# Kernel tuning notes

Hardware: AMD Instinct MI355X
Metric: run time of the kernel (lower is better)

## Reference

```python
import jax, jax.numpy as jnp
import numpy as np

HOP = jnp.array([0, 1, 4, 7, 2, 5, 8, 3, 6, 9, 11, 14, 10, 12, 15, 13, 16])
GRAPH = jnp.array([0, 1, 4, 7, 2, 5, 8, 3, 6, 9, 12, 10, 13, 15, 11, 14, 16])
D_MODEL, L, D_INNER, D_STATE, DT_RANK = 512, 17, 1024, 4, 32


def layernorm(x, w, b, eps=1e-5):
    mu = x.mean(-1, keepdims=True)
    var = ((x - mu) ** 2).mean(-1, keepdims=True)
    return (x - mu) * jax.lax.rsqrt(var + eps) * w + b


def setup_inputs() -> dict:
    key = jax.random.key(0)
    ks = jax.random.split(key, 9)
    B = 4096
    s = lambda k, shape: jax.random.normal(k, shape, jnp.float32) * 0.02
    # A_log init per mamba_ssm: log(1..d_state) repeated over d_inner
    A_log = jnp.log(jnp.broadcast_to(jnp.arange(1, D_STATE + 1, dtype=jnp.float32), (D_INNER, D_STATE)))
    return {
        "x": jax.random.normal(ks[0], (B, L, D_MODEL), jnp.float32),
        "bp_embed": s(ks[1], (1, 5, D_MODEL)),
        "ln_w": jnp.ones((D_MODEL,), jnp.float32),
        "ln_b": jnp.zeros((D_MODEL,), jnp.float32),
        "in_proj_w": s(ks[2], (2 * D_INNER, D_MODEL)),
        "conv_w": 1.0 + s(ks[3], (D_INNER,)),  # d_conv=1 depthwise conv == per-channel scale
        "conv_b": jnp.zeros((D_INNER,), jnp.float32),
        "x_proj_w": s(ks[4], (DT_RANK + 2 * D_STATE, D_INNER)),
        "dt_proj_w": s(ks[5], (D_INNER, DT_RANK)),
        "dt_proj_b": s(ks[6], (D_INNER,)) - 4.0,  # softplus-inverse-ish small dt init
        "A_log": A_log,
        "D": jnp.ones((D_INNER,), jnp.float32),
        "out_proj_w": s(ks[7], (D_MODEL, D_INNER)),
    }


def mamba(u, in_proj_w, conv_w, conv_b, x_proj_w, dt_proj_w, dt_proj_b, A_log, D, out_proj_w):
    # u: [B, L, d_model]
    xz = jnp.einsum('bld,ed->ble', u, in_proj_w)          # [B,L,2*d_inner]
    xm, z = jnp.split(xz, 2, axis=-1)
    xm = jax.nn.silu(xm * conv_w + conv_b)                 # d_conv=1 -> pointwise
    x_dbl = jnp.einsum('ble,fe->blf', xm, x_proj_w)        # [B,L,dt_rank+2*d_state]
    dt_r = x_dbl[..., :DT_RANK]
    Bm = x_dbl[..., DT_RANK:DT_RANK + D_STATE]
    Cm = x_dbl[..., DT_RANK + D_STATE:]
    dt = jax.nn.softplus(jnp.einsum('blr,er->ble', dt_r, dt_proj_w) + dt_proj_b)  # [B,L,d_inner]
    A = -jnp.exp(A_log)                                    # [d_inner,d_state]

    def step(h, inp):
        dt_t, B_t, C_t, x_t = inp                          # [B,di],[B,ds],[B,ds],[B,di]
        dA = jnp.exp(dt_t[..., None] * A)                  # [B,di,ds]
        h = dA * h + (dt_t * x_t)[..., None] * B_t[:, None, :]
        y = jnp.einsum('bes,bs->be', h, C_t)
        return h, y

    bsz = u.shape[0]
    h0 = jnp.zeros((bsz, D_INNER, D_STATE), u.dtype)
    seq = (dt.transpose(1, 0, 2), Bm.transpose(1, 0, 2), Cm.transpose(1, 0, 2), xm.transpose(1, 0, 2))
    _, ys = jax.lax.scan(step, h0, seq)                    # ys: [L,B,d_inner]
    y = ys.transpose(1, 0, 2) + xm * D
    y = y * jax.nn.silu(z)
    return jnp.einsum('ble,de->bld', y, out_proj_w)


def reference(x, bp_embed, ln_w, ln_b, in_proj_w, conv_w, conv_b, x_proj_w,
              dt_proj_w, dt_proj_b, A_log, D, out_proj_w):
    bp = bp_embed
    x_bpe = jnp.concatenate([bp[:, :3], bp[:, :3], bp[:, :3], bp[:, :1],
                             bp[:, 3:], bp[:, :1], bp[:, 3:], bp[:, 3:]], axis=1)  # [1,17,dim]
    x_ssm = x[:, HOP, :] + x_bpe
    x_ssm = layernorm(x_ssm, ln_w, ln_b)
    x_ssm = mamba(x_ssm, in_proj_w, conv_w, conv_b, x_proj_w,
                  dt_proj_w, dt_proj_b, A_log, D, out_proj_w)
    return x + x_ssm[:, GRAPH, :]
```

## Files before the change

### kernel.cpp

```cpp
#include <hip/hip_runtime.h>

typedef unsigned short u16;
typedef unsigned int   u32;
typedef __bf16 bf16_t;
typedef bf16_t bf16x8 __attribute__((ext_vector_type(8)));
typedef float  f32x4  __attribute__((ext_vector_type(4)));

#define DEV static __device__ __forceinline__

__constant__ int c_HOP[17] = {0,1,4,7,2,5,8,3,6,9,11,14,10,12,15,13,16};
__constant__ int c_BPE[17] = {0,1,2,0,1,2,0,1,2,0,3,4,0,3,4,3,4};

DEV u16 f2bf(float f){
  u32 x = __builtin_bit_cast(u32, f);
  x += 0x7fffu + ((x >> 16) & 1u);
  return (u16)(x >> 16);
}
DEV float bf2f(u32 u){ return __builtin_bit_cast(float, u << 16); }
DEV float silu_f(float v){ return v / (1.f + __expf(-v)); }

DEV void gll16(const void* g, void* l){
  __builtin_amdgcn_global_load_lds((__attribute__((address_space(1))) void*)g,
                                   (__attribute__((address_space(3))) void*)l,
                                   16, 0, 0);
}

__global__ __launch_bounds__(256) void cvt4(
    const float* __restrict__ s0, u16* __restrict__ d0, int n0,
    const float* __restrict__ s1, u16* __restrict__ d1, int n1,
    const float* __restrict__ s2, u16* __restrict__ d2, int n2,
    const float* __restrict__ s3, u16* __restrict__ d3, int n3)
{
  int t = blockIdx.x * 256 + threadIdx.x;
  if (t < n0){ d0[t] = f2bf(s0[t]); return; }
  t -= n0; if (t < n1){ d1[t] = f2bf(s1[t]); return; }
  t -= n1; if (t < n2){ d2[t] = f2bf(s2[t]); return; }
  t -= n2; if (t < n3){ d3[t] = f2bf(s3[t]); }
}

__global__ __launch_bounds__(256) void ln_gather(
    const float* __restrict__ x, const float* __restrict__ bpe,
    const float* __restrict__ lnw, const float* __restrict__ lnb,
    u16* __restrict__ u)
{
  int tok = blockIdx.x;
  int b = tok / 17;
  int l = tok - b * 17;
  const float* xr = x   + ((size_t)b * 17 + c_HOP[l]) * 512;
  const float* br = bpe + (size_t)c_BPE[l] * 512;
  int tid = threadIdx.x;
  int d0 = tid * 2;
  float2 xv = *(const float2*)(xr + d0);
  float2 bv = *(const float2*)(br + d0);
  float v0 = xv.x + bv.x, v1 = xv.y + bv.y;

  __shared__ float red[8];
  float s = v0 + v1;
  #pragma unroll
  for (int o = 32; o; o >>= 1) s += __shfl_xor(s, o);
  if ((tid & 63) == 0) red[tid >> 6] = s;
  __syncthreads();
  float mu = (red[0] + red[1] + red[2] + red[3]) * (1.f / 512.f);
  float a0 = v0 - mu, a1 = v1 - mu;
  float q = a0 * a0 + a1 * a1;
  #pragma unroll
  for (int o = 32; o; o >>= 1) q += __shfl_xor(q, o);
  if ((tid & 63) == 0) red[4 + (tid >> 6)] = q;
  __syncthreads();
  float var = (red[4] + red[5] + red[6] + red[7]) * (1.f / 512.f);
  float rs = rsqrtf(var + 1e-5f);

  u16 o0 = f2bf(a0 * rs * lnw[d0]     + lnb[d0]);
  u16 o1 = f2bf(a1 * rs * lnw[d0 + 1] + lnb[d0 + 1]);
  u32 pack = (u32)o0 | ((u32)o1 << 16);
  *(u32*)(u + (size_t)tok * 512 + d0) = pack;
}

enum { EPI_SPLIT = 0, EPI_XDBL = 1, EPI_DT = 2, EPI_OUT = 3 };

template<int EPI>
__global__ __launch_bounds__(256) void gemm_bt(
    const u16* __restrict__ A, int lda,
    const u16* __restrict__ W, int nW, int K, int MT,
    u16* __restrict__ ob0, u16* __restrict__ ob1,
    const float* __restrict__ p0, const float* __restrict__ p1,
    const float* __restrict__ xres, float* __restrict__ fout)
{
  __shared__ u16 sA[128 * 32];
  __shared__ u16 sW[128 * 32];
  int bid = blockIdx.x;
  int mt = bid % MT, nt = bid / MT;
  int brow = mt * 128, bcol = nt * 128;
  int tid = threadIdx.x, lane = tid & 63, wid = tid >> 6;
  int wm = wid >> 1, wn = wid & 1;

  f32x4 acc[4][4] = {};

  int srow = tid >> 2;
  int sch  = tid & 3;

  for (int kt = 0; kt < K; kt += 32) {
    #pragma unroll
    for (int i = 0; i < 2; i++) {
      int r = i * 64 + srow;
      int c = sch ^ ((r >> 1) & 3);
      gll16(A + (size_t)(brow + r) * lda + kt + c * 8,
            (char*)sA + tid * 16 + i * 4096);
    }
    #pragma unroll
    for (int i = 0; i < 2; i++) {
      int r = i * 64 + srow;
      int wr = bcol + r; wr = (wr < nW) ? wr : 0;
      int c = sch ^ ((r >> 1) & 3);
      gll16(W + (size_t)wr * K + kt + c * 8,
            (char*)sW + tid * 16 + i * 4096);
    }
    __syncthreads();

    bf16x8 av[4], bv[4];
    #pragma unroll
    for (int mi = 0; mi < 4; mi++) {
      int r = wm * 64 + mi * 16 + (lane & 15);
      int c = (lane >> 4) ^ ((r >> 1) & 3);
      av[mi] = *(const bf16x8*)((const char*)sA + r * 64 + c * 16);
    }
    #pragma unroll
    for (int ni = 0; ni < 4; ni++) {
      int r = wn * 64 + ni * 16 + (lane & 15);
      int c = (lane >> 4) ^ ((r >> 1) & 3);
      bv[ni] = *(const bf16x8*)((const char*)sW + r * 64 + c * 16);
    }
    #pragma unroll
    for (int mi = 0; mi < 4; mi++)
      #pragma unroll
      for (int ni = 0; ni < 4; ni++)
        acc[mi][ni] = __builtin_amdgcn_mfma_f32_16x16x32_bf16(
            av[mi], bv[ni], acc[mi][ni], 0, 0, 0);
    __syncthreads();
  }

  int r4 = (lane >> 4) * 4;
  int cl = lane & 15;
  #pragma unroll
  for (int mi = 0; mi < 4; mi++) {
    #pragma unroll
    for (int ni = 0; ni < 4; ni++) {
      int col = bcol + wn * 64 + ni * 16 + cl;
      if (col >= nW) continue;
      #pragma unroll
      for (int rr = 0; rr < 4; rr++) {
        int row = brow + wm * 64 + mi * 16 + r4 + rr;
        float v = acc[mi][ni][rr];
        if constexpr (EPI == EPI_SPLIT) {
          if (col < 1024) {
            float t = v * p0[col] + p1[col];
            ob0[(size_t)row * 1024 + col] = f2bf(silu_f(t));
          } else {
            ob1[(size_t)row * 1024 + (col - 1024)] = f2bf(silu_f(v));
          }
        } else if constexpr (EPI == EPI_XDBL) {
          ob0[(size_t)row * 40 + col] = f2bf(v);
        } else if constexpr (EPI == EPI_DT) {
          float s = v + p0[col];
          float dtv = (s > 20.f) ? s : log1pf(__expf(s));
          ob0[(size_t)row * 1024 + col] = f2bf(dtv);
        } else {
          u32 rw = (u32)row;
          u32 b = rw / 17u;
          int gl = (int)(rw - b * 17u);
          size_t oi = ((size_t)b * 17 + c_HOP[gl]) * 512 + col;
          fout[oi] = xres[oi] + v;
        }
      }
    }
  }
}

__global__ __launch_bounds__(256) void scan_k(
    const u16* __restrict__ xm, const u16* __restrict__ zs,
    const u16* __restrict__ xdbl, u16* __restrict__ dty,
    const float* __restrict__ A_log, const float* __restrict__ Dp)
{
  int gid = blockIdx.x * 256 + threadIdx.x;
  int b = gid >> 10, e = gid & 1023;
  float A0 = -__expf(A_log[e * 4 + 0]);
  float A1 = -__expf(A_log[e * 4 + 1]);
  float A2 = -__expf(A_log[e * 4 + 2]);
  float A3 = -__expf(A_log[e * 4 + 3]);
  float Dv = Dp[e];
  float h0 = 0.f, h1 = 0.f, h2 = 0.f, h3 = 0.f;
  size_t base = (size_t)b * 17;
  for (int t = 0; t < 17; t++) {
    size_t tok = base + t;
    size_t idx = tok * 1024 + e;
    float dt = bf2f(dty[idx]);
    float xv = bf2f(xm[idx]);
    float zv = bf2f(zs[idx]);
    uint4 raw = *(const uint4*)(xdbl + tok * 40 + 32);
    float B0 = bf2f(raw.x & 0xffffu), B1 = bf2f(raw.x >> 16);
    float B2 = bf2f(raw.y & 0xffffu), B3 = bf2f(raw.y >> 16);
    float C0 = bf2f(raw.z & 0xffffu), C1 = bf2f(raw.z >> 16);
    float C2 = bf2f(raw.w & 0xffffu), C3 = bf2f(raw.w >> 16);
    float dx = dt * xv;
    h0 = __expf(dt * A0) * h0 + dx * B0;
    h1 = __expf(dt * A1) * h1 + dx * B1;
    h2 = __expf(dt * A2) * h2 + dx * B2;
    h3 = __expf(dt * A3) * h3 + dx * B3;
    float y = h0 * C0 + h1 * C1 + h2 * C2 + h3 * C3;
    dty[idx] = f2bf((y + xv * Dv) * zv);
  }
}

extern "C" void kernel_launch(void* const* d_in, const int* in_sizes, int n_in,
                              void* d_out, int out_size, void* d_ws, size_t ws_size,
                              hipStream_t stream) {
  const float* x     = (const float*)d_in[0];
  const float* bpe   = (const float*)d_in[1];
  const float* lnw   = (const float*)d_in[2];
  const float* lnb   = (const float*)d_in[3];
  const float* w_in  = (const float*)d_in[4];
  const float* convw = (const float*)d_in[5];
  const float* convb = (const float*)d_in[6];
  const float* w_xp  = (const float*)d_in[7];
  const float* w_dt  = (const float*)d_in[8];
  const float* b_dt  = (const float*)d_in[9];
  const float* A_log = (const float*)d_in[10];
  const float* Dp    = (const float*)d_in[11];
  const float* w_out = (const float*)d_in[12];
  float* out = (float*)d_out;

  u16* ws = (u16*)d_ws;
  u16* wb_in  = ws;
  u16* wb_out = wb_in  + 1048576;
  u16* wb_xp  = wb_out + 524288;
  u16* wb_dt  = wb_xp  + 40960;
  u16* xm     = wb_dt  + 32768;
  u16* zs     = xm     + 71303168;
  u16* xdbl   = zs     + 71303168;
  u16* dty    = xdbl   + 2785280;
  u16* u      = dty;

  const int MT = 544;

  cvt4<<<6432, 256, 0, stream>>>(w_in, wb_in, 1048576, w_out, wb_out, 524288,
                                 w_xp, wb_xp, 40960, w_dt, wb_dt, 32768);

  ln_gather<<<69632, 256, 0, stream>>>(x, bpe, lnw, lnb, u);

  gemm_bt<EPI_SPLIT><<<MT * 16, 256, 0, stream>>>(
      u, 512, wb_in, 2048, 512, MT, xm, zs, convw, convb, nullptr, nullptr);

  gemm_bt<EPI_XDBL><<<MT * 1, 256, 0, stream>>>(
      xm, 1024, wb_xp, 40, 1024, MT, xdbl, nullptr, nullptr, nullptr, nullptr, nullptr);

  gemm_bt<EPI_DT><<<MT * 8, 256, 0, stream>>>(
      xdbl, 40, wb_dt, 1024, 32, MT, dty, nullptr, b_dt, nullptr, nullptr, nullptr);

  scan_k<<<16384, 256, 0, stream>>>(xm, zs, xdbl, dty, A_log, Dp);

  gemm_bt<EPI_OUT><<<MT * 4, 256, 0, stream>>>(
      dty, 1024, wb_out, 512, 1024, MT, nullptr, nullptr, nullptr, nullptr, x, out);
}
```

Measured before the change: 962.8 us.

## Fuse x_proj, dt_proj and selective scan into per-batch kernel; remap GEMM blocks

Replaces the separate x_proj GEMM, dt_proj GEMM and scan kernels with one per-batch-row kernel. It computes x_dbl with MFMA, keeps x_dbl and dt in shared memory, then runs the scan, so the large dt tensor never goes through global memory. The remaining GEMMs get an XCD-aware block index remap (blockIdx&7 striping, with the n tile varying fastest). The SPLIT epilogue now packs two bf16 outputs per 32-bit store using a lane shuffle. Risks: the fused kernel uses about 53KB of LDS per block, which limits occupancy, and its x_proj loads read straight from global memory with no tiling.

```diff
diff --git a/kernel.cpp b/kernel.cpp
--- a/kernel.cpp
+++ b/kernel.cpp
@@ -76,20 +76,23 @@
   *(u32*)(u + (size_t)tok * 512 + d0) = pack;
 }
 
-enum { EPI_SPLIT = 0, EPI_XDBL = 1, EPI_DT = 2, EPI_OUT = 3 };
+enum { EPI_SPLIT = 0, EPI_OUT = 1 };
 
 template<int EPI>
 __global__ __launch_bounds__(256) void gemm_bt(
     const u16* __restrict__ A, int lda,
-    const u16* __restrict__ W, int nW, int K, int MT,
+    const u16* __restrict__ W, int K, int MT,
     u16* __restrict__ ob0, u16* __restrict__ ob1,
     const float* __restrict__ p0, const float* __restrict__ p1,
     const float* __restrict__ xres, float* __restrict__ fout)
 {
   __shared__ u16 sA[128 * 32];
   __shared__ u16 sW[128 * 32];
-  int bid = blockIdx.x;
-  int mt = bid % MT, nt = bid / MT;
+  int nwg = gridDim.x;
+  int cpx = nwg >> 3;
+  int wg = (blockIdx.x & 7) * cpx + (blockIdx.x >> 3);
+  int NT = nwg / MT;
+  int nt = wg % NT, mt = wg / NT;
   int brow = mt * 128, bcol = nt * 128;
   int tid = threadIdx.x, lane = tid & 63, wid = tid >> 6;
   int wm = wid >> 1, wn = wid & 1;
@@ -110,9 +113,8 @@
     #pragma unroll
     for (int i = 0; i < 2; i++) {
       int r = i * 64 + srow;
-      int wr = bcol + r; wr = (wr < nW) ? wr : 0;
       int c = sch ^ ((r >> 1) & 3);
-      gll16(W + (size_t)wr * K + kt + c * 8,
+      gll16(W + (size_t)(bcol + r) * K + kt + c * 8,
             (char*)sW + tid * 16 + i * 4096);
     }
     __syncthreads();
@@ -143,71 +145,156 @@
   int cl = lane & 15;
   #pragma unroll
   for (int mi = 0; mi < 4; mi++) {
+    int rowb = brow + wm * 64 + mi * 16 + r4;
     #pragma unroll
     for (int ni = 0; ni < 4; ni++) {
       int col = bcol + wn * 64 + ni * 16 + cl;
-      if (col >= nW) continue;
-      #pragma unroll
-      for (int rr = 0; rr < 4; rr++) {
-        int row = brow + wm * 64 + mi * 16 + r4 + rr;
-        float v = acc[mi][ni][rr];
-        if constexpr (EPI == EPI_SPLIT) {
-          if (col < 1024) {
-            float t = v * p0[col] + p1[col];
-            ob0[(size_t)row * 1024 + col] = f2bf(silu_f(t));
-          } else {
-            ob1[(size_t)row * 1024 + (col - 1024)] = f2bf(silu_f(v));
+      if constexpr (EPI == EPI_SPLIT) {
+        bool isx = (col < 1024);
+        float cw = isx ? p0[col] : 1.f;
+        float cb = isx ? p1[col] : 0.f;
+        float rv[4];
+        #pragma unroll
+        for (int rr = 0; rr < 4; rr++)
+          rv[rr] = silu_f(acc[mi][ni][rr] * cw + cb);
+        #pragma unroll
+        for (int rr = 0; rr < 4; rr++) {
+          float ov = __shfl_xor(rv[rr], 1);
+          if (!(lane & 1)) {
+            u32 pk = (u32)f2bf(rv[rr]) | ((u32)f2bf(ov) << 16);
+            size_t rowoff = (size_t)(rowb + rr) * 1024;
+            if (isx) *(u32*)(ob0 + rowoff + col) = pk;
+            else     *(u32*)(ob1 + rowoff + (col - 1024)) = pk;
           }
-        } else if constexpr (EPI == EPI_XDBL) {
-          ob0[(size_t)row * 40 + col] = f2bf(v);
-        } else if constexpr (EPI == EPI_DT) {
-          float s = v + p0[col];
-          float dtv = (s > 20.f) ? s : log1pf(__expf(s));
-          ob0[(size_t)row * 1024 + col] = f2bf(dtv);
-        } else {
+        }
+      } else {
+        #pragma unroll
+        for (int rr = 0; rr < 4; rr++) {
+          int row = rowb + rr;
           u32 rw = (u32)row;
           u32 b = rw / 17u;
           int gl = (int)(rw - b * 17u);
           size_t oi = ((size_t)b * 17 + c_HOP[gl]) * 512 + col;
-          fout[oi] = xres[oi] + v;
+          fout[oi] = xres[oi] + acc[mi][ni][rr];
         }
       }
     }
   }
 }
 
-__global__ __launch_bounds__(256) void scan_k(
+__global__ __launch_bounds__(256) void mamba_mid(
     const u16* __restrict__ xm, const u16* __restrict__ zs,
-    const u16* __restrict__ xdbl, u16* __restrict__ dty,
-    const float* __restrict__ A_log, const float* __restrict__ Dp)
+    const u16* __restrict__ wxp, const u16* __restrict__ wdt,
+    const float* __restrict__ bdt, const float* __restrict__ A_log,
+    const float* __restrict__ Dp, u16* __restrict__ y)
 {
-  int gid = blockIdx.x * 256 + threadIdx.x;
-  int b = gid >> 10, e = gid & 1023;
-  float A0 = -__expf(A_log[e * 4 + 0]);
-  float A1 = -__expf(A_log[e * 4 + 1]);
-  float A2 = -__expf(A_log[e * 4 + 2]);
-  float A3 = -__expf(A_log[e * 4 + 3]);
-  float Dv = Dp[e];
-  float h0 = 0.f, h1 = 0.f, h2 = 0.f, h3 = 0.f;
-  size_t base = (size_t)b * 17;
-  for (int t = 0; t < 17; t++) {
-    size_t tok = base + t;
-    size_t idx = tok * 1024 + e;
-    float dt = bf2f(dty[idx]);
-    float xv = bf2f(xm[idx]);
-    float zv = bf2f(zs[idx]);
-    uint4 raw = *(const uint4*)(xdbl + tok * 40 + 32);
-    float B0 = bf2f(raw.x & 0xffffu), B1 = bf2f(raw.x >> 16);
-    float B2 = bf2f(raw.y & 0xffffu), B3 = bf2f(raw.y >> 16);
-    float C0 = bf2f(raw.z & 0xffffu), C1 = bf2f(raw.z >> 16);
-    float C2 = bf2f(raw.w & 0xffffu), C3 = bf2f(raw.w >> 16);
-    float dx = dt * xv;
-    h0 = __expf(dt * A0) * h0 + dx * B0;
-    h1 = __expf(dt * A1) * h1 + dx * B1;
-    h2 = __expf(dt * A2) * h2 + dx * B2;
-    h3 = __expf(dt * A3) * h3 + dx * B3;
-    float y = h0 * C0 + h1 * C1 + h2 * C2 + h3 * C3;
-    dty[idx] = f2bf((y + xv * Dv) * zv);
+  __shared__ float part[4][17][52];
+  __shared__ float xdbl_s[17][52];
+  __shared__ u16 dt_s[17][1032];
+
+  int b = blockIdx.x;
+  int tid = threadIdx.x, lane = tid & 63, wid = tid >> 6;
+  int l15 = lane & 15, lhi = lane >> 4;
+  const size_t base = (size_t)b * 17 * 1024;
+
+  {
+    f32x4 acc1[2][3] = {};
+    int k0 = wid * 256;
+    for (int ks = 0; ks < 8; ks++) {
+      int kk = k0 + ks * 32 + lhi * 8;
+      bf16x8 a0 = *(const bf16x8*)(xm + base + (size_t)l15 * 1024 + kk);
+      bf16x8 a1 = *(const bf16x8*)(xm + base + (size_t)16  * 1024 + kk);
+      #pragma unroll
+      for (int nf = 0; nf < 3; nf++) {
+        int f = nf * 16 + l15; f = (f < 40) ? f : 39;
+        bf16x8 bv = *(const bf16x8*)(wxp + (size_t)f * 1024 + kk);
+        acc1[0][nf] = __builtin_amdgcn_mfma_f32_16x16x32_bf16(a0, bv, acc1[0][nf], 0,0,0);
+        acc1[1][nf] = __builtin_amdgcn_mfma_f32_16x16x32_bf16(a1, bv, acc1[1][nf], 0,0,0);
+      }
+    }
+    #pragma unroll
+    for (int mi = 0; mi < 2; mi++)
+      #pragma unroll
+      for (int nf = 0; nf < 3; nf++)
+        #pragma unroll
+        for (int rr = 0; rr < 4; rr++) {
+          int row = mi * 16 + lhi * 4 + rr;
+          if (row < 17) part[wid][row][nf * 16 + l15] = acc1[mi][nf][rr];
+        }
+  }
+  __syncthreads();
+  for (int i = tid; i < 17 * 48; i += 256) {
+    int t = i / 48, c = i - t * 48;
+    xdbl_s[t][c] = part[0][t][c] + part[1][t][c] + part[2][t][c] + part[3][t][c];
+  }
+  __syncthreads();
+
+  {
+    bf16x8 a2_0, a2_1;
+    int kk2 = lhi * 8;
+    #pragma unroll
+    for (int j = 0; j < 8; j++) {
+      a2_0[j] = (bf16_t)xdbl_s[l15][kk2 + j];
+      a2_1[j] = (bf16_t)xdbl_s[16][kk2 + j];
+    }
+    #pragma unroll
+    for (int half = 0; half < 2; half++) {
+      f32x4 acc2[2][8] = {};
+      #pragma unroll
+      for (int nf = 0; nf < 8; nf++) {
+        int e = (wid * 16 + half * 8 + nf) * 16 + l15;
+        bf16x8 bv = *(const bf16x8*)(wdt + (size_t)e * 32 + kk2);
+        acc2[0][nf] = __builtin_amdgcn_mfma_f32_16x16x32_bf16(a2_0, bv, acc2[0][nf], 0,0,0);
+        acc2[1][nf] = __builtin_amdgcn_mfma_f32_16x16x32_bf16(a2_1, bv, acc2[1][nf], 0,0,0);
+      }
+      #pragma unroll
+      for (int nf = 0; nf < 8; nf++) {
+        int e = (wid * 16 + half * 8 + nf) * 16 + l15;
+        float bb = bdt[e];
+        #pragma unroll
+        for (int mi = 0; mi < 2; mi++)
+          #pragma unroll
+          for (int rr = 0; rr < 4; rr++) {
+            int t = mi * 16 + lhi * 4 + rr;
+            if (t < 17) {
+              float s = acc2[mi][nf][rr] + bb;
+              float d = (s > 20.f) ? s : log1pf(__expf(s));
+              dt_s[t][e] = f2bf(d);
+            }
+          }
+      }
+    }
+  }
+  __syncthreads();
+
+  const u16* xmb = xm + base;
+  const u16* zsb = zs + base;
+  u16* yb = y + base;
+  for (int c = 0; c < 4; c++) {
+    int e = c * 256 + tid;
+    float4 al = *(const float4*)(A_log + (size_t)e * 4);
+    float Av0 = -__expf(al.x), Av1 = -__expf(al.y);
+    float Av2 = -__expf(al.z), Av3 = -__expf(al.w);
+    float Dv = Dp[e];
+    float h0 = 0.f, h1 = 0.f, h2 = 0.f, h3 = 0.f;
+    #pragma unroll
+    for (int t = 0; t < 17; t++) {
+      int off = t * 1024 + e;
+      float dtv = bf2f(dt_s[t][e]);
+      float xv = bf2f(xmb[off]);
+      float zv = bf2f(zsb[off]);
+      float B0 = xdbl_s[t][32], B1 = xdbl_s[t][33];
+      float B2 = xdbl_s[t][34], B3 = xdbl_s[t][35];
+      float C0 = xdbl_s[t][36], C1 = xdbl_s[t][37];
+      float C2 = xdbl_s[t][38], C3 = xdbl_s[t][39];
+      float dx = dtv * xv;
+      h0 = __expf(dtv * Av0) * h0 + dx * B0;
+      h1 = __expf(dtv * Av1) * h1 + dx * B1;
+      h2 = __expf(dtv * Av2) * h2 + dx * B2;
+      h3 = __expf(dtv * Av3) * h3 + dx * B3;
+      float yv = h0 * C0 + h1 * C1 + h2 * C2 + h3 * C3;
+      yb[off] = f2bf((yv + xv * Dv) * zv);
+    }
   }
 }
 
@@ -236,9 +323,8 @@
   u16* wb_dt  = wb_xp  + 40960;
   u16* xm     = wb_dt  + 32768;
   u16* zs     = xm     + 71303168;
-  u16* xdbl   = zs     + 71303168;
-  u16* dty    = xdbl   + 2785280;
-  u16* u      = dty;
+  u16* yv     = zs     + 71303168;
+  u16* u      = yv;
 
   const int MT = 544;
 
@@ -248,16 +334,10 @@
   ln_gather<<<69632, 256, 0, stream>>>(x, bpe, lnw, lnb, u);
 
   gemm_bt<EPI_SPLIT><<<MT * 16, 256, 0, stream>>>(
-      u, 512, wb_in, 2048, 512, MT, xm, zs, convw, convb, nullptr, nullptr);
-
-  gemm_bt<EPI_XDBL><<<MT * 1, 256, 0, stream>>>(
-      xm, 1024, wb_xp, 40, 1024, MT, xdbl, nullptr, nullptr, nullptr, nullptr, nullptr);
-
-  gemm_bt<EPI_DT><<<MT * 8, 256, 0, stream>>>(
-      xdbl, 40, wb_dt, 1024, 32, MT, dty, nullptr, b_dt, nullptr, nullptr, nullptr);
-
-  scan_k<<<16384, 256, 0, stream>>>(xm, zs, xdbl, dty, A_log, Dp);
+      u, 512, wb_in, 512, MT, xm, zs, convw, convb, nullptr, nullptr);
+
+  mamba_mid<<<4096, 256, 0, stream>>>(xm, zs, wb_xp, wb_dt, b_dt, A_log, Dp, yv);
 
   gemm_bt<EPI_OUT><<<MT * 4, 256, 0, stream>>>(
-      dty, 1024, wb_out, 512, 1024, MT, nullptr, nullptr, nullptr, nullptr, x, out);
-}
+      yv, 1024, wb_out, 1024, MT, nullptr, nullptr, nullptr, nullptr, x, out);
+}
```

After: 1.218 ms. +26.5%, slower.
